# Kernel tuning notes

Measured on AMD Instinct MI355X. Metric: run time of the kernel, lower is better.

Reference implementation:

```python
import jax, jax.numpy as jnp
import numpy as np


def setup_inputs() -> dict:
    key = jax.random.key(0)
    k1, k2 = jax.random.split(key)
    z = jax.random.normal(k1, (16, 256, 64, 64), dtype=jnp.float32)
    # codebook initialized uniform(-1/size, 1/size) in the original; values don't
    # affect the math path, use same distribution for realism
    size, code_dim = 1024, 256
    weight = jax.random.uniform(k2, (size, code_dim), dtype=jnp.float32,
                                minval=-1.0 / size, maxval=1.0 / size)
    return {"z": z, "weight": weight}


def reference(z, weight):
    b, c, h, w = z.shape  # c == code_dim
    flat = jnp.transpose(z, (0, 2, 3, 1)).reshape(-1, c)  # [N, D]
    # squared L2 distances via ||a-b||^2 = ||a||^2 - 2 a.b + ||b||^2
    d = (jnp.sum(flat * flat, axis=1, keepdims=True)
         - 2.0 * flat @ weight.T
         + jnp.sum(weight * weight, axis=1))  # [N, size]
    encoding_indices = jnp.argmin(d, axis=-1).reshape(b, h, w)  # int indices
    quantized = jnp.transpose(weight[encoding_indices], (0, 3, 1, 2))  # [b,c,h,w]
    straight_through = jax.lax.stop_gradient(quantized - z) + z
    return quantized, straight_through, encoding_indices
```

## Files before the change

### kernel.cpp

```cpp
#include <hip/hip_runtime.h>


#define NROWS 65536
#define DDIM 256
#define KCODES 1024
#define TAU 2e-4f
#define WWIN 2e-4f

typedef unsigned long long u64;
typedef _Float16 f16x8 __attribute__((ext_vector_type(8)));
typedef float f32x4 __attribute__((ext_vector_type(4)));

__device__ __forceinline__ void gld16(const void* g, void* l) {
    __builtin_amdgcn_global_load_lds((const __attribute__((address_space(1))) void*)g,
                                     (__attribute__((address_space(3))) void*)l, 16, 0, 0);
}

template <typename F>
__device__ __forceinline__ float np_pairwise256_sq(F get) {
    float half[2];
#pragma unroll
    for (int h = 0; h < 2; ++h) {
        float r[8];
#pragma unroll
        for (int j = 0; j < 8; ++j) { float v = get(h * 128 + j); r[j] = __fmul_rn(v, v); }
        for (int i = 8; i < 128; i += 8)
#pragma unroll
            for (int j = 0; j < 8; ++j) {
                float v = get(h * 128 + i + j);
                r[j] = __fadd_rn(r[j], __fmul_rn(v, v));
            }
        half[h] = __fadd_rn(__fadd_rn(__fadd_rn(r[0], r[1]), __fadd_rn(r[2], r[3])),
                            __fadd_rn(__fadd_rn(r[4], r[5]), __fadd_rn(r[6], r[7])));
    }
    return __fadd_rn(half[0], half[1]);
}

__global__ void prep_w_k(const float* __restrict__ w, f16x8* __restrict__ w16,
                         float* __restrict__ wn) {
    int bid = blockIdx.x;
    if (bid < 128) {
        int idx = bid * 256 + threadIdx.x;
        int o = idx >> 10, c = idx & 1023;
        const float* wp = w + (size_t)c * DDIM + o * 8;
        f16x8 hv;
#pragma unroll
        for (int j = 0; j < 8; ++j) hv[j] = (_Float16)(wp[j] * 1024.0f);
        w16[(size_t)o * 1024 + c] = hv;
    } else {
        int k = (bid - 128) * 256 + threadIdx.x;
        const float* wp = w + (size_t)k * DDIM;
        wn[k] = np_pairwise256_sq([&](int i) { return wp[i]; });
    }
}

#define DPP_MIN(CTRL) {                                                                 \
    float ov = __int_as_float(__builtin_amdgcn_mov_dpp(__float_as_int(bv), CTRL, 0xf, 0xf, false)); \
    bv = fminf(bv, ov); }

__device__ __forceinline__ int aswz(int row) {
    return (row * 16) ^ (((row >> 2) & 7) << 4);
}

__launch_bounds__(256, 2)
__global__ void argmin_fused_k(const float* __restrict__ z, const f16x8* __restrict__ w16,
                               const float* __restrict__ wn,
                               float* __restrict__ btv, u64* __restrict__ bmk) {
    __shared__ char arena[81920];
    char* lA = arena;
    char* lB = arena + 65536;
    const int t = threadIdx.x;
    const int lane = t & 63;
    const int l15 = lane & 15, l4 = lane >> 4;
    const int wid = t >> 6;
    const int wm = wid >> 1, wn_ = wid & 1;
    const int n0 = blockIdx.x * 128;
    const float* zb = z + (size_t)(n0 >> 12) * 1048576 + (n0 & 4095);

    auto STAGE_B = [&](int cb, int s, int buf) {
#pragma unroll
        for (int q = 0; q < 2; ++q) {
            int i = wid * 2 + q;
            int o = s * 4 + (i >> 1);
            int half = i & 1;
            gld16(w16 + (size_t)(o * 1024 + cb * 128 + half * 64 + lane),
                  lB + buf * 8192 + i * 1024);
        }
    };
    STAGE_B(0, 0, 0);

    {
        int oc = t >> 5;
        int rq = t & 31;
#pragma unroll
        for (int p = 0; p < 4; ++p) {
            int o = p * 8 + oc;
            float4 L[8];
#pragma unroll
            for (int j = 0; j < 8; ++j)
                L[j] = *reinterpret_cast<const float4*>(zb + (size_t)(o * 8 + j) * 4096 + rq * 4);
#pragma unroll
            for (int k = 0; k < 4; ++k) {
                f16x8 rec;
#pragma unroll
                for (int j = 0; j < 8; ++j) {
                    const float* lj = reinterpret_cast<const float*>(&L[j]);
                    rec[j] = (_Float16)lj[k];
                }
                *reinterpret_cast<f16x8*>(lA + o * 2048 + aswz(rq * 4 + k)) = rec;
            }
        }
    }
    __syncthreads();

    auto COMPUTE = [&](int s, int buf, f32x4 (&acc)[4][4]) {
        f16x8 a[4], b[4];
        const char* pb = lB + buf * 8192 + l4 * 2048 + (wn_ * 64 + l15) * 16;
#pragma unroll
        for (int nt = 0; nt < 4; ++nt) b[nt] = *reinterpret_cast<const f16x8*>(pb + nt * 256);
        const char* pa = lA + (s * 4 + l4) * 2048;
#pragma unroll
        for (int mt = 0; mt < 4; ++mt)
            a[mt] = *reinterpret_cast<const f16x8*>(pa + aswz(wm * 64 + mt * 16 + l15));
#pragma unroll
        for (int mt = 0; mt < 4; ++mt)
#pragma unroll
            for (int nt = 0; nt < 4; ++nt)
                acc[mt][nt] = __builtin_amdgcn_mfma_f32_16x16x32_f16(a[mt], b[nt], acc[mt][nt], 0, 0, 0);
    };

#pragma unroll 1
    for (int cb = 0; cb < 8; ++cb) {
        f32x4 acc[4][4];
#pragma unroll
        for (int mt = 0; mt < 4; ++mt)
#pragma unroll
            for (int nt = 0; nt < 4; ++nt) acc[mt][nt] = f32x4{0.f, 0.f, 0.f, 0.f};

#pragma unroll
        for (int s = 0; s < 8; ++s) {
            if (s < 7)       STAGE_B(cb, s + 1, (s + 1) & 1);
            else if (cb < 7) STAGE_B(cb + 1, 0, 0);
            if (s == 7 && cb == 7) { asm volatile("s_waitcnt vmcnt(0)" ::: "memory"); }
            else                   { asm volatile("s_waitcnt vmcnt(2)" ::: "memory"); }
            __builtin_amdgcn_s_barrier();
            COMPUTE(s, s & 1, acc);
            __builtin_amdgcn_s_barrier();
        }

        const int c0 = cb << 7;
        float wnv[4];
#pragma unroll
        for (int nt = 0; nt < 4; ++nt) wnv[nt] = wn[c0 + wn_ * 64 + nt * 16 + l15];
        const int ebase = ((cb << 1) | wn_) << 16;
#pragma unroll
        for (int mt = 0; mt < 4; ++mt) {
#pragma unroll
            for (int r = 0; r < 4; ++r) {
                float s0 = fmaf(-0.001953125f, acc[mt][0][r], wnv[0]);
                float s1 = fmaf(-0.001953125f, acc[mt][1][r], wnv[1]);
                float s2 = fmaf(-0.001953125f, acc[mt][2][r], wnv[2]);
                float s3 = fmaf(-0.001953125f, acc[mt][3][r], wnv[3]);
                float bv = fminf(fminf(s0, s1), fminf(s2, s3));
                DPP_MIN(0xB1)
                DPP_MIN(0x4E)
                DPP_MIN(0x141)
                DPP_MIN(0x140)
                float thr = bv + WWIN;
                u64 b0 = __ballot(s0 < thr), b1 = __ballot(s1 < thr);
                u64 b2 = __ballot(s2 < thr), b3 = __ballot(s3 < thr);
                int sh = 16 * l4;
                u64 msk = ((b0 >> sh) & 0xFFFFull)
                        | (((b1 >> sh) & 0xFFFFull) << 16)
                        | (((b2 >> sh) & 0xFFFFull) << 32)
                        | (((b3 >> sh) & 0xFFFFull) << 48);
                if (l15 == 0) {
                    int row = wm * 64 + mt * 16 + l4 * 4 + r;
                    btv[ebase + n0 + row] = bv;
                    bmk[ebase + n0 + row] = msk;
                }
            }
        }
    }
}

__global__ void finrescue_k(const float* __restrict__ z, const float* __restrict__ w,
                            const float* __restrict__ s2,
                            const float* __restrict__ btv, const u64* __restrict__ bmk,
                            float* __restrict__ idxf_out) {
    __shared__ float zsh[16][256];
    const int lane = threadIdx.x;
    const int n0 = blockIdx.x * 16;
    const int r = lane >> 2;
    const int eq = lane & 3;
    const int n = n0 + r;

    float bv = 3.4e38f, b2 = 3.4e38f;
    int be = 0;
#pragma unroll
    for (int i = 0; i < 4; ++i) {
        int e = eq * 4 + i;
        float v = btv[(e << 16) + n];
        if (v < bv) { b2 = bv; bv = v; be = e; }
        else b2 = fminf(b2, v);
    }
#pragma unroll
    for (int m = 1; m < 4; m <<= 1) {
        float ov = __shfl_xor(bv, m), o2 = __shfl_xor(b2, m);
        int oe = __shfl_xor(be, m);
        if (ov < bv || (ov == bv && oe < be)) { b2 = fminf(bv, o2); bv = ov; be = oe; }
        else b2 = fminf(b2, ov);
    }
    u64 wmask = bmk[((u64)be << 16) + n];
    int bi = be * 64 + (int)(__ffsll((long long)wmask) - 1);
    bool flag = (__popcll(wmask) > 1) || (b2 - bv < TAU);
    if (eq == 0) idxf_out[n] = (float)bi;
    u64 fb = __ballot(flag);
    if ((fb & 0x1111111111111111ull) == 0) return;

    const float* zb = z + (size_t)(n0 >> 12) * 1048576 + (n0 & 4095);
#pragma unroll
    for (int it = 0; it < 16; ++it) {
        int d = it * 16 + (lane >> 2);
        float4 v = *reinterpret_cast<const float4*>(zb + (size_t)d * 4096 + (lane & 3) * 4);
        zsh[(lane & 3) * 4 + 0][d] = v.x;
        zsh[(lane & 3) * 4 + 1][d] = v.y;
        zsh[(lane & 3) * 4 + 2][d] = v.z;
        zsh[(lane & 3) * 4 + 3][d] = v.w;
    }
    __syncthreads();

    for (int r2 = 0; r2 < 16; ++r2) {
        if (!((fb >> (r2 * 4)) & 1)) continue;
        int nn = n0 + r2;
        int hh = (lane >> 3) & 1, jj = lane & 7;
        float v0 = zsh[r2][hh * 128 + jj];
        float accj = __fmul_rn(v0, v0);
#pragma unroll
        for (int i = 1; i < 16; ++i) {
            float v2 = zsh[r2][hh * 128 + i * 8 + jj];
            accj = __fadd_rn(accj, __fmul_rn(v2, v2));
        }
        float a1 = __fadd_rn(accj, __shfl_xor(accj, 1));
        float a2 = __fadd_rn(a1, __shfl_xor(a1, 2));
        float a4 = __fadd_rn(a2, __shfl_xor(a2, 4));
        float s1 = __fadd_rn(a4, __shfl_xor(a4, 8));

        float gv = __shfl(bv, r2 * 4);

        float zr0 = zsh[r2][lane * 4 + 0], zr1 = zsh[r2][lane * 4 + 1];
        float zr2 = zsh[r2][lane * 4 + 2], zr3 = zsh[r2][lane * 4 + 3];
        float bv2 = 3.4e38f;
        int   bi2 = 0;
        for (int e = 0; e < 16; ++e) {
            float tv = btv[(e << 16) + nn];
            if (tv <= gv + TAU) {
                u64 m = bmk[((u64)e << 16) + nn];
                while (m) {
                    int k = __ffsll((long long)m) - 1;
                    m &= m - 1;
                    int c = e * 64 + k;
                    const float* wp = w + (size_t)c * DDIM + lane * 4;
                    double md = 0.0;
                    md = fma((double)zr0, (double)wp[0], md);
                    md = fma((double)zr1, (double)wp[1], md);
                    md = fma((double)zr2, (double)wp[2], md);
                    md = fma((double)zr3, (double)wp[3], md);
#pragma unroll
                    for (int mm = 1; mm < 64; mm <<= 1) md += __shfl_xor(md, mm);
                    float dq = __fadd_rn((float)((double)s1 - 2.0 * md), s2[c]);
                    if (dq < bv2) { bv2 = dq; bi2 = c; }
                }
            }
        }
        if (lane == 0) idxf_out[nn] = (float)bi2;
    }
}

__global__ void gather_k(const float* __restrict__ idxf, const float* __restrict__ w,
                         float* __restrict__ out0, float* __restrict__ out1) {
    int tid = blockIdx.x * 256 + threadIdx.x;
    int n   = tid & 65535;
    int c4  = tid >> 16;
    int code = (int)idxf[n];
    float4 v = *reinterpret_cast<const float4*>(w + (size_t)code * DDIM + c4 * 4);
    size_t off = (size_t)(n >> 12) * 1048576 + (size_t)c4 * 4 * 4096 + (n & 4095);
    out0[off]         = v.x;
    out0[off + 4096]  = v.y;
    out0[off + 8192]  = v.z;
    out0[off + 12288] = v.w;
    out1[off]         = v.x;
    out1[off + 4096]  = v.y;
    out1[off + 8192]  = v.z;
    out1[off + 12288] = v.w;
}

extern "C" void kernel_launch(void* const* d_in, const int* in_sizes, int n_in,
                              void* d_out, int out_size, void* d_ws, size_t ws_size,
                              hipStream_t stream) {
    const float* z = (const float*)d_in[0];
    const float* w = (const float*)d_in[1];
    float* out    = (float*)d_out;
    float* out0   = out;
    float* out1   = out + 16777216;
    float* outidx = out + 33554432;

    char* s1b = (char*)out1;
    f16x8* w16 = (f16x8*)s1b;
    float* wn  = (float*)(s1b + 1048576);
    float* btv = (float*)(s1b + 2097152);
    u64*   bmk = (u64*)(s1b + 10485760);

    prep_w_k<<<132, 256, 0, stream>>>(w, w16, wn);
    argmin_fused_k<<<NROWS / 128, 256, 0, stream>>>(z, w16, wn, btv, bmk);
    finrescue_k<<<NROWS / 16, 64, 0, stream>>>(z, w, wn, btv, bmk, outidx);
    gather_k<<<NROWS * 64 / 256, 256, 0, stream>>>(outidx, w, out0, out1);
}
```

Measured before the change: 111.5 us.

## Swizzle block order and pack four rescue waves per block with ballot-based candidate filtering

The argmin kernel now maps blocks to rows through an XCD-aware swizzle. The rescue kernel runs four independent 64-lane waves per 256-thread block, each with its own padded shared-memory slice, so the block-wide barrier becomes a per-wave lgkmcnt wait. The per-row threshold test that used to reload btv inside the rescue loop is replaced by ballots of values already held in registers, and the z row load is vectorised. These changes aim to cut redundant global loads, launch and scheduling overhead for tiny blocks, and cross-XCD L2 locality loss. The cost is more shared memory per block.

```diff
diff --git a/kernel.cpp b/kernel.cpp
--- a/kernel.cpp
+++ b/kernel.cpp
@@ -74,7 +74,8 @@
     const int l15 = lane & 15, l4 = lane >> 4;
     const int wid = t >> 6;
     const int wm = wid >> 1, wn_ = wid & 1;
-    const int n0 = blockIdx.x * 128;
+    const int p = blockIdx.x;
+    const int n0 = (((p & 7) << 6) | (p >> 3)) << 7;
     const float* zb = z + (size_t)(n0 >> 12) * 1048576 + (n0 & 4095);
 
     auto STAGE_B = [&](int cb, int s, int buf) {
@@ -93,8 +94,8 @@
         int oc = t >> 5;
         int rq = t & 31;
 #pragma unroll
-        for (int p = 0; p < 4; ++p) {
-            int o = p * 8 + oc;
+        for (int p2 = 0; p2 < 4; ++p2) {
+            int o = p2 * 8 + oc;
             float4 L[8];
 #pragma unroll
             for (int j = 0; j < 8; ++j)
@@ -184,25 +185,33 @@
     }
 }
 
+__launch_bounds__(256, 2)
 __global__ void finrescue_k(const float* __restrict__ z, const float* __restrict__ w,
                             const float* __restrict__ s2,
                             const float* __restrict__ btv, const u64* __restrict__ bmk,
                             float* __restrict__ idxf_out) {
-    __shared__ float zsh[16][256];
-    const int lane = threadIdx.x;
-    const int n0 = blockIdx.x * 16;
+    __shared__ float zsh[4][16][260];
+    const int t = threadIdx.x;
+    const int lane = t & 63;
+    const int wid = t >> 6;
+    const int p = blockIdx.x;
+    const int grp = (((p & 7) << 7) | (p >> 3)) * 4 + wid;
+    const int n0 = grp * 16;
     const int r = lane >> 2;
     const int eq = lane & 3;
     const int n = n0 + r;
 
+    float v0 = btv[((eq * 4 + 0) << 16) + n];
+    float v1 = btv[((eq * 4 + 1) << 16) + n];
+    float v2 = btv[((eq * 4 + 2) << 16) + n];
+    float v3 = btv[((eq * 4 + 3) << 16) + n];
     float bv = 3.4e38f, b2 = 3.4e38f;
     int be = 0;
-#pragma unroll
-    for (int i = 0; i < 4; ++i) {
-        int e = eq * 4 + i;
-        float v = btv[(e << 16) + n];
-        if (v < bv) { b2 = bv; bv = v; be = e; }
-        else b2 = fminf(b2, v);
+    {
+        if (v0 < bv) { b2 = bv; bv = v0; be = eq * 4 + 0; } else b2 = fminf(b2, v0);
+        if (v1 < bv) { b2 = bv; bv = v1; be = eq * 4 + 1; } else b2 = fminf(b2, v1);
+        if (v2 < bv) { b2 = bv; bv = v2; be = eq * 4 + 2; } else b2 = fminf(b2, v2);
+        if (v3 < bv) { b2 = bv; bv = v3; be = eq * 4 + 3; } else b2 = fminf(b2, v3);
     }
 #pragma unroll
     for (int m = 1; m < 4; m <<= 1) {
@@ -215,6 +224,12 @@
     int bi = be * 64 + (int)(__ffsll((long long)wmask) - 1);
     bool flag = (__popcll(wmask) > 1) || (b2 - bv < TAU);
     if (eq == 0) idxf_out[n] = (float)bi;
+
+    u64 bal0 = __ballot(v0 <= bv + TAU);
+    u64 bal1 = __ballot(v1 <= bv + TAU);
+    u64 bal2 = __ballot(v2 <= bv + TAU);
+    u64 bal3 = __ballot(v3 <= bv + TAU);
+
     u64 fb = __ballot(flag);
     if ((fb & 0x1111111111111111ull) == 0) return;
 
@@ -223,38 +238,38 @@
     for (int it = 0; it < 16; ++it) {
         int d = it * 16 + (lane >> 2);
         float4 v = *reinterpret_cast<const float4*>(zb + (size_t)d * 4096 + (lane & 3) * 4);
-        zsh[(lane & 3) * 4 + 0][d] = v.x;
-        zsh[(lane & 3) * 4 + 1][d] = v.y;
-        zsh[(lane & 3) * 4 + 2][d] = v.z;
-        zsh[(lane & 3) * 4 + 3][d] = v.w;
-    }
-    __syncthreads();
-
+        zsh[wid][(lane & 3) * 4 + 0][d] = v.x;
+        zsh[wid][(lane & 3) * 4 + 1][d] = v.y;
+        zsh[wid][(lane & 3) * 4 + 2][d] = v.z;
+        zsh[wid][(lane & 3) * 4 + 3][d] = v.w;
+    }
+    asm volatile("s_waitcnt lgkmcnt(0)" ::: "memory");
+    __builtin_amdgcn_sched_barrier(0);
+
+#pragma unroll 1
     for (int r2 = 0; r2 < 16; ++r2) {
         if (!((fb >> (r2 * 4)) & 1)) continue;
         int nn = n0 + r2;
         int hh = (lane >> 3) & 1, jj = lane & 7;
-        float v0 = zsh[r2][hh * 128 + jj];
-        float accj = __fmul_rn(v0, v0);
+        float w0 = zsh[wid][r2][hh * 128 + jj];
+        float accj = __fmul_rn(w0, w0);
 #pragma unroll
         for (int i = 1; i < 16; ++i) {
-            float v2 = zsh[r2][hh * 128 + i * 8 + jj];
-            accj = __fadd_rn(accj, __fmul_rn(v2, v2));
+            float w2 = zsh[wid][r2][hh * 128 + i * 8 + jj];
+            accj = __fadd_rn(accj, __fmul_rn(w2, w2));
         }
         float a1 = __fadd_rn(accj, __shfl_xor(accj, 1));
         float a2 = __fadd_rn(a1, __shfl_xor(a1, 2));
         float a4 = __fadd_rn(a2, __shfl_xor(a2, 4));
         float s1 = __fadd_rn(a4, __shfl_xor(a4, 8));
 
-        float gv = __shfl(bv, r2 * 4);
-
-        float zr0 = zsh[r2][lane * 4 + 0], zr1 = zsh[r2][lane * 4 + 1];
-        float zr2 = zsh[r2][lane * 4 + 2], zr3 = zsh[r2][lane * 4 + 3];
+        float4 zr4 = *reinterpret_cast<const float4*>(&zsh[wid][r2][lane * 4]);
         float bv2 = 3.4e38f;
         int   bi2 = 0;
+#pragma unroll
         for (int e = 0; e < 16; ++e) {
-            float tv = btv[(e << 16) + nn];
-            if (tv <= gv + TAU) {
+            u64 bal = (e & 3) == 0 ? bal0 : (e & 3) == 1 ? bal1 : (e & 3) == 2 ? bal2 : bal3;
+            if ((bal >> (r2 * 4 + (e >> 2))) & 1) {
                 u64 m = bmk[((u64)e << 16) + nn];
                 while (m) {
                     int k = __ffsll((long long)m) - 1;
@@ -262,10 +277,10 @@
                     int c = e * 64 + k;
                     const float* wp = w + (size_t)c * DDIM + lane * 4;
                     double md = 0.0;
-                    md = fma((double)zr0, (double)wp[0], md);
-                    md = fma((double)zr1, (double)wp[1], md);
-                    md = fma((double)zr2, (double)wp[2], md);
-                    md = fma((double)zr3, (double)wp[3], md);
+                    md = fma((double)zr4.x, (double)wp[0], md);
+                    md = fma((double)zr4.y, (double)wp[1], md);
+                    md = fma((double)zr4.z, (double)wp[2], md);
+                    md = fma((double)zr4.w, (double)wp[3], md);
 #pragma unroll
                     for (int mm = 1; mm < 64; mm <<= 1) md += __shfl_xor(md, mm);
                     float dq = __fadd_rn((float)((double)s1 - 2.0 * md), s2[c]);
@@ -313,6 +328,6 @@
 
     prep_w_k<<<132, 256, 0, stream>>>(w, w16, wn);
     argmin_fused_k<<<NROWS / 128, 256, 0, stream>>>(z, w16, wn, btv, bmk);
-    finrescue_k<<<NROWS / 16, 64, 0, stream>>>(z, w, wn, btv, bmk, outidx);
+    finrescue_k<<<NROWS / 64, 256, 0, stream>>>(z, w, wn, btv, bmk, outidx);
     gather_k<<<NROWS * 64 / 256, 256, 0, stream>>>(outidx, w, out0, out1);
 }
```

Result: faster. 106.1 us (-4.8%).
